# Kernel optimization log

Hardware: AMD Instinct MI355X
Metric: run time of the kernel (lower is better)

Reference implementation:

```python
import jax, jax.numpy as jnp
import numpy as np

B, N, D, OUT = 32, 4096, 512, 512
LN_EPS = 1e-5
EPS = 1e-8


def _layernorm(x, g, b):
    m = jnp.mean(x, axis=-1, keepdims=True)
    v = jnp.mean((x - m) ** 2, axis=-1, keepdims=True)
    return (x - m) * jax.lax.rsqrt(v + LN_EPS) * g + b


def setup_inputs() -> dict:
    key = jax.random.key(0)
    ks = jax.random.split(key, 12)
    x = jax.random.normal(ks[0], (B, N, D), dtype=jnp.float32)
    mask = jax.random.bernoulli(ks[1], 0.9, (B, N))
    mask = mask.at[:, 0].set(True)  # guarantee no fully-masked row
    h = D // 4
    s = lambda fan_in: 1.0 / np.sqrt(fan_in)
    return {
        "x": x,
        "mask": mask,
        # attention MLP: Linear(D, D//4) -> tanh -> Linear(D//4, 1)
        "attn_w1": jax.random.normal(ks[2], (D, h), jnp.float32) * s(D),
        "attn_b1": jnp.zeros((h,), jnp.float32),
        "attn_w2": jax.random.normal(ks[3], (h, 1), jnp.float32) * s(h),
        "attn_b2": jnp.zeros((1,), jnp.float32),
        # gate: Linear(3D, D) -> LN -> GELU -> Linear(D, 3) -> softmax
        "gate_w1": jax.random.normal(ks[4], (3 * D, D), jnp.float32) * s(3 * D),
        "gate_b1": jnp.zeros((D,), jnp.float32),
        "gate_ln_g": jnp.ones((D,), jnp.float32),
        "gate_ln_b": jnp.zeros((D,), jnp.float32),
        "gate_w2": jax.random.normal(ks[5], (D, 3), jnp.float32) * s(D),
        "gate_b2": jnp.zeros((3,), jnp.float32),
        # out_proj: Linear(D, OUT) -> LN -> Dropout(eval: identity)
        "out_w": jax.random.normal(ks[6], (D, OUT), jnp.float32) * s(D),
        "out_b": jnp.zeros((OUT,), jnp.float32),
        "out_ln_g": jnp.ones((OUT,), jnp.float32),
        "out_ln_b": jnp.zeros((OUT,), jnp.float32),
    }


def reference(x, mask, attn_w1, attn_b1, attn_w2, attn_b2,
              gate_w1, gate_b1, gate_ln_g, gate_ln_b, gate_w2, gate_b2,
              out_w, out_b, out_ln_g, out_ln_b):
    # attention scores: [B, N]
    h = jnp.tanh(jnp.einsum('bnd,dh->bnh', x, attn_w1) + attn_b1)
    scores = (jnp.einsum('bnh,ho->bno', h, attn_w2) + attn_b2)[..., 0]
    scores = jnp.where(mask, scores, -jnp.inf)
    attn_w = jax.nn.softmax(scores, axis=-1)
    attn_w = jnp.nan_to_num(attn_w, nan=0.0)
    attn_pooled = jnp.einsum('bnd,bn->bd', x, attn_w)

    # masked max pool
    x_masked = jnp.where(mask[..., None], x, -jnp.inf)
    max_pooled = jnp.max(x_masked, axis=1)
    max_pooled = jnp.nan_to_num(max_pooled, nan=0.0, posinf=0.0, neginf=0.0)

    # masked mean pool
    mfl = mask.astype(x.dtype)
    masked_sum = jnp.einsum('bnd,bn->bd', x, mfl)
    num_valid = jnp.clip(jnp.sum(mfl, axis=1, keepdims=True), EPS, None)
    mean_pooled = masked_sum / num_valid

    # gated combine
    combined = jnp.concatenate([attn_pooled, max_pooled, mean_pooled], axis=-1)
    g = combined @ gate_w1 + gate_b1
    g = _layernorm(g, gate_ln_g, gate_ln_b)
    g = jax.nn.gelu(g, approximate=False)
    gates = jax.nn.softmax(g @ gate_w2 + gate_b2, axis=-1)  # [B, 3]

    stacked = jnp.stack([attn_pooled, max_pooled, mean_pooled], axis=2)  # [B, D, 3]
    weighted = jnp.einsum('bdk,bk->bd', stacked, gates)

    out = weighted @ out_w + out_b
    out = _layernorm(out, out_ln_g, out_ln_b)  # dropout: eval mode -> identity
    return out
```

## Files before the change

### kernel.cpp

```cpp
#include <hip/hip_runtime.h>
#include <hip/hip_bf16.h>
#include <math.h>

#define BB 32
#define NN 4096
#define DD 512
#define HH 128
#define NCH 128
#define LN_EPS 1e-5f
#define MEPS 1e-8f

typedef __attribute__((ext_vector_type(8))) short bf16x8;
typedef __attribute__((ext_vector_type(4))) float f32x4;

__device__ __forceinline__ unsigned pk_bf16(float a, float b) {
    unsigned ua = __float_as_uint(a); ua = (ua + 0x7FFFu + ((ua >> 16) & 1u)) >> 16;
    unsigned ub = __float_as_uint(b); ub = (ub + 0x7FFFu + ((ub >> 16) & 1u)) >> 16;
    return ua | (ub << 16);
}
__device__ __forceinline__ unsigned short bf16_1(float a) {
    unsigned ua = __float_as_uint(a);
    return (unsigned short)((ua + 0x7FFFu + ((ua >> 16) & 1u)) >> 16);
}
__device__ __forceinline__ float bflo(unsigned u) { return __uint_as_float(u << 16); }
__device__ __forceinline__ float bfhi(unsigned u) { return __uint_as_float(u & 0xFFFF0000u); }

__global__ __launch_bounds__(256) void gmsp_prep(
    const void* __restrict__ mask, unsigned char* __restrict__ m8,
    const float* __restrict__ w1, unsigned short* __restrict__ w1f)
{
    int blk = blockIdx.x, t = threadIdx.x;
    if (blk < 512) {
        __shared__ int sf[2];
        const unsigned* mu = (const unsigned*)mask;
        bool f32f = false, i8f = false;
#pragma unroll
        for (int i = 0; i < 4; ++i) {
            unsigned v = mu[t + i * 256];
            f32f |= (v == 0x3F800000u);
            i8f  |= (v > 1u) && (v != 0x3F800000u);
        }
        if (t == 0) { sf[0] = 0; sf[1] = 0; }
        __syncthreads();
        int wf32 = __any((int)f32f), wi8 = __any((int)i8f);
        if ((t & 63) == 0) {
            if (wf32) atomicOr(&sf[0], 1);
            if (wi8)  atomicOr(&sf[1], 1);
        }
        __syncthreads();
        int fmt = sf[0] ? 2 : (sf[1] ? 1 : 0);
        int i = blk * 256 + t;
        unsigned char v;
        if (fmt == 1)      v = ((const unsigned char*)mask)[i] != 0;
        else if (fmt == 2) v = ((const float*)mask)[i] != 0.0f;
        else               v = ((const int*)mask)[i] != 0;
        m8[i] = v;
    } else {
        int idx = (blk - 512) * 256 + t;
        int j = idx & 7;
        int e = idx >> 3;
        int lane = e & 63;
        int half = (e >> 6) & 1;
        int s = (e >> 7) & 15;
        int g2 = (e >> 11) & 3;
        int h = g2 * 32 + half * 16 + (lane & 15);
        int k = s * 32 + (lane >> 4) * 8 + j;
        w1f[(size_t)e * 8 + j] = bf16_1(w1[(size_t)k * HH + h]);
    }
}

__global__ __launch_bounds__(256, 4) void gmsp_fused(
    const float* __restrict__ x, const unsigned short* __restrict__ w1f,
    const float* __restrict__ b1, const float* __restrict__ w2,
    const float* __restrict__ b2, const unsigned char* __restrict__ m8,
    float* __restrict__ attnp, float* __restrict__ sump, float* __restrict__ maxp,
    float* __restrict__ mc, float* __restrict__ sc, float* __restrict__ cnt)
{
    __shared__ char At[32 * 1024];
    __shared__ float sred[32][4] __attribute__((aligned(16)));
    __shared__ float wrow[32];
    __shared__ float cpool[2][512];

    const int t = threadIdx.x;
    const int lane = t & 63, wid = t >> 6;
    const int l15 = lane & 15, lq = (lane >> 4) & 3;
    const int blk = blockIdx.x;
    const int b = blk >> 7, ch = blk & 127;
    const size_t row0 = (size_t)b * NN + (size_t)ch * 32;

    float4 sreg[16];
    {
        const float4* xb = (const float4*)(x + row0 * DD);
#pragma unroll
        for (int j = 0; j < 16; ++j) sreg[j] = xb[j * 256 + t];
    }
    uint4 mq0 = *(const uint4*)(m8 + row0);
    uint4 mq1 = *(const uint4*)(m8 + row0 + 16);
    unsigned mwa[8] = {mq0.x, mq0.y, mq0.z, mq0.w, mq1.x, mq1.y, mq1.z, mq1.w};

    const int H = t >> 7;
    const int c4 = t & 127;
    float ps[4] = {0.f, 0.f, 0.f, 0.f};
    float pm[4] = {-INFINITY, -INFINITY, -INFINITY, -INFINITY};
#pragma unroll
    for (int j = 0; j < 16; ++j) {
        const int row = 2 * j + H;
        float4 v = sreg[j];
        uint2 pw; pw.x = pk_bf16(v.x, v.y); pw.y = pk_bf16(v.z, v.w);
        *(uint2*)(At + row * 1024 + ((c4 * 8) ^ ((row & 7) << 4))) = pw;
        int mv = (mwa[j >> 1] >> ((2 * (j & 1) + H) * 8)) & 0xFF;
        if (mv) {
            ps[0] += v.x; ps[1] += v.y; ps[2] += v.z; ps[3] += v.w;
            pm[0] = fmaxf(pm[0], v.x); pm[1] = fmaxf(pm[1], v.y);
            pm[2] = fmaxf(pm[2], v.z); pm[3] = fmaxf(pm[3], v.w);
        }
    }
    __syncthreads();

    const int hb = wid * 32;
    f32x4 acc00 = (f32x4)0.f, acc01 = (f32x4)0.f, acc10 = (f32x4)0.f, acc11 = (f32x4)0.f;
    {
        const char* wf = (const char*)w1f + (size_t)wid * 32768 + (size_t)lane * 16;
        const char* ar0 = At + l15 * 1024;
        const char* ar1 = At + (16 + l15) * 1024;
        const int swz = (l15 & 7) << 4;
#pragma unroll
        for (int s = 0; s < 16; ++s) {
            bf16x8 bf0 = *(const bf16x8*)(wf + s * 2048);
            bf16x8 bf1 = *(const bf16x8*)(wf + s * 2048 + 1024);
            const int co = (s * 64 + lq * 16) ^ swz;
            bf16x8 a0 = *(const bf16x8*)(ar0 + co);
            bf16x8 a1 = *(const bf16x8*)(ar1 + co);
            acc00 = __builtin_amdgcn_mfma_f32_16x16x32_bf16(a0, bf0, acc00, 0, 0, 0);
            acc01 = __builtin_amdgcn_mfma_f32_16x16x32_bf16(a0, bf1, acc01, 0, 0, 0);
            acc10 = __builtin_amdgcn_mfma_f32_16x16x32_bf16(a1, bf0, acc10, 0, 0, 0);
            acc11 = __builtin_amdgcn_mfma_f32_16x16x32_bf16(a1, bf1, acc11, 0, 0, 0);
        }
    }
    {
        const float b10 = b1[hb + l15], b11 = b1[hb + 16 + l15];
        const float w20 = w2[hb + l15], w21 = w2[hb + 16 + l15];
#pragma unroll
        for (int rf = 0; rf < 2; ++rf) {
            f32x4 aA = rf ? acc10 : acc00;
            f32x4 aB = rf ? acc11 : acc01;
#pragma unroll
            for (int r = 0; r < 4; ++r) {
                float p0 = fminf(fmaxf(aA[r] + b10, -10.f), 10.f);
                float p1 = fminf(fmaxf(aB[r] + b11, -10.f), 10.f);
                float e0 = __expf(2.f * p0), e1 = __expf(2.f * p1);
                float v = (e0 - 1.f) / (e0 + 1.f) * w20 + (e1 - 1.f) / (e1 + 1.f) * w21;
                v += __shfl_xor(v, 1); v += __shfl_xor(v, 2);
                v += __shfl_xor(v, 4); v += __shfl_xor(v, 8);
                if (l15 == 0) sred[rf * 16 + lq * 4 + r][wid] = v;
            }
        }
    }
    __syncthreads();

    if (t < 32) {
        float4 s4 = *(const float4*)&sred[t][0];
        float ssum = s4.x + s4.y + s4.z + s4.w + b2[0];
        int valid = m8[row0 + t];
        float score = valid ? ssum : -INFINITY;
        float mx = score;
        mx = fmaxf(mx, __shfl_xor(mx, 1));  mx = fmaxf(mx, __shfl_xor(mx, 2));
        mx = fmaxf(mx, __shfl_xor(mx, 4));  mx = fmaxf(mx, __shfl_xor(mx, 8));
        mx = fmaxf(mx, __shfl_xor(mx, 16));
        float e = valid ? __expf(score - mx) : 0.f;
        wrow[t] = e;
        float ts = e, tc = valid ? 1.f : 0.f;
        ts += __shfl_xor(ts, 1);  tc += __shfl_xor(tc, 1);
        ts += __shfl_xor(ts, 2);  tc += __shfl_xor(tc, 2);
        ts += __shfl_xor(ts, 4);  tc += __shfl_xor(tc, 4);
        ts += __shfl_xor(ts, 8);  tc += __shfl_xor(tc, 8);
        ts += __shfl_xor(ts, 16); tc += __shfl_xor(tc, 16);
        if (t == 0) { mc[blk] = mx; sc[blk] = ts; cnt[blk] = tc; }
    }
    __syncthreads();

    float a0 = 0.f, a1 = 0.f;
#pragma unroll 8
    for (int r = 0; r < 32; ++r) {
        float w = wrow[r];
        unsigned u = *(const unsigned*)(At + r * 1024 + ((t * 4) ^ ((r & 7) << 4)));
        a0 = fmaf(w, bflo(u), a0);
        a1 = fmaf(w, bfhi(u), a1);
    }

    *(float4*)&cpool[H][c4 * 4] = make_float4(ps[0], ps[1], ps[2], ps[3]);
    __syncthreads();
    float sv0 = cpool[0][2 * t] + cpool[1][2 * t];
    float sv1 = cpool[0][2 * t + 1] + cpool[1][2 * t + 1];
    __syncthreads();
    *(float4*)&cpool[H][c4 * 4] = make_float4(pm[0], pm[1], pm[2], pm[3]);
    __syncthreads();
    float mv0 = fmaxf(cpool[0][2 * t], cpool[1][2 * t]);
    float mv1 = fmaxf(cpool[0][2 * t + 1], cpool[1][2 * t + 1]);

    const size_t ob = (size_t)blk * DD + 2 * t;
    *(float2*)(attnp + ob) = make_float2(a0, a1);
    *(float2*)(sump + ob)  = make_float2(sv0, sv1);
    *(float2*)(maxp + ob)  = make_float2(mv0, mv1);
}

__device__ __forceinline__ float gmsp_bsum(float v, float* red, int t) {
    __syncthreads();
    red[t] = v; __syncthreads();
    for (int s = 256; s > 0; s >>= 1) { if (t < s) red[t] += red[t + s]; __syncthreads(); }
    return red[0];
}
__device__ __forceinline__ float gmsp_bmax(float v, float* red, int t) {
    __syncthreads();
    red[t] = v; __syncthreads();
    for (int s = 256; s > 0; s >>= 1) { if (t < s) red[t] = fmaxf(red[t], red[t + s]); __syncthreads(); }
    return red[0];
}

__global__ __launch_bounds__(512) void gmsp_tail(
    const float* __restrict__ attnp, const float* __restrict__ sump,
    const float* __restrict__ maxp, const float* __restrict__ mc,
    const float* __restrict__ sc, const float* __restrict__ cnt,
    const float* __restrict__ gate_w1, const float* __restrict__ gate_b1,
    const float* __restrict__ gln_g, const float* __restrict__ gln_b,
    const float* __restrict__ gate_w2, const float* __restrict__ gate_b2,
    const float* __restrict__ out_w, const float* __restrict__ out_b,
    const float* __restrict__ oln_g, const float* __restrict__ oln_b,
    float* __restrict__ out)
{
    __shared__ float comb[3 * DD];
    __shared__ float wvec[DD];
    __shared__ float red[512];
    __shared__ float ef[NCH];
    __shared__ float part[4][DD];
    int b = blockIdx.x, t = threadIdx.x;

    float mcv = (t < NCH) ? mc[b * NCH + t] : -INFINITY;
    float M = gmsp_bmax(mcv, red, t);
    float e = (t < NCH && mcv != -INFINITY) ? __expf(mcv - M) : 0.f;
    if (t < NCH) ef[t] = e;
    float T = gmsp_bsum(e * ((t < NCH) ? sc[b * NCH + t] : 0.f), red, t);
    float C = gmsp_bsum((t < NCH) ? cnt[b * NCH + t] : 0.f, red, t);
    float invT = T > 0.f ? 1.f / T : 0.f;
    C = fmaxf(C, MEPS);
    __syncthreads();

    float ax = 0.f, sx = 0.f, mx = -INFINITY;
    for (int c = 0; c < NCH; ++c) {
        size_t base = (size_t)(b * NCH + c) * DD + t;
        ax = fmaf(ef[c], attnp[base], ax);
        sx += sump[base];
        mx = fmaxf(mx, maxp[base]);
    }
    ax *= invT;
    float meanx = sx / C;
    if (isinf(mx)) mx = 0.f;

    comb[t] = ax;
    comb[DD + t] = mx;
    comb[2 * DD + t] = meanx;
    __syncthreads();

    const int th = t & 127, kh = t >> 7;
    {
        float4 g4 = make_float4(0.f, 0.f, 0.f, 0.f);
        const float* gw = gate_w1 + (size_t)kh * 384 * DD + th * 4;
        for (int k = 0; k < 384; ++k) {
            float cv = comb[kh * 384 + k];
            float4 wv = *(const float4*)(gw + (size_t)k * DD);
            g4.x = fmaf(cv, wv.x, g4.x); g4.y = fmaf(cv, wv.y, g4.y);
            g4.z = fmaf(cv, wv.z, g4.z); g4.w = fmaf(cv, wv.w, g4.w);
        }
        *(float4*)&part[kh][th * 4] = g4;
    }
    __syncthreads();
    float gx = part[0][t] + part[1][t] + part[2][t] + part[3][t] + gate_b1[t];

    float mg = gmsp_bsum(gx, red, t) * (1.f / DD);
    float vg = gmsp_bsum(gx * gx, red, t) * (1.f / DD) - mg * mg;
    float inv = rsqrtf(vg + LN_EPS);
    gx = (gx - mg) * inv * gln_g[t] + gln_b[t];
    gx = 0.5f * gx * (1.f + erff(gx * 0.70710678118654752f));

    float l0 = gmsp_bsum(gx * gate_w2[t * 3 + 0], red, t) + gate_b2[0];
    float l1 = gmsp_bsum(gx * gate_w2[t * 3 + 1], red, t) + gate_b2[1];
    float l2 = gmsp_bsum(gx * gate_w2[t * 3 + 2], red, t) + gate_b2[2];
    float mxl = fmaxf(l0, fmaxf(l1, l2));
    float e0 = __expf(l0 - mxl), e1 = __expf(l1 - mxl), e2 = __expf(l2 - mxl);
    float ie = 1.f / (e0 + e1 + e2);
    float gw0 = e0 * ie, gw1 = e1 * ie, gw2 = e2 * ie;

    wvec[t] = ax * gw0 + mx * gw1 + meanx * gw2;
    __syncthreads();

    {
        float4 o4 = make_float4(0.f, 0.f, 0.f, 0.f);
        const float* ow = out_w + (size_t)kh * 128 * DD + th * 4;
        for (int k = 0; k < 128; ++k) {
            float wvk = wvec[kh * 128 + k];
            float4 w4 = *(const float4*)(ow + (size_t)k * DD);
            o4.x = fmaf(wvk, w4.x, o4.x); o4.y = fmaf(wvk, w4.y, o4.y);
            o4.z = fmaf(wvk, w4.z, o4.z); o4.w = fmaf(wvk, w4.w, o4.w);
        }
        *(float4*)&part[kh][th * 4] = o4;
    }
    __syncthreads();
    float ox = part[0][t] + part[1][t] + part[2][t] + part[3][t] + out_b[t];

    float mo = gmsp_bsum(ox, red, t) * (1.f / DD);
    float vo = gmsp_bsum(ox * ox, red, t) * (1.f / DD) - mo * mo;
    float io = rsqrtf(vo + LN_EPS);
    out[(size_t)b * DD + t] = (ox - mo) * io * oln_g[t] + oln_b[t];
}

extern "C" void kernel_launch(void* const* d_in, const int* in_sizes, int n_in,
                              void* d_out, int out_size, void* d_ws, size_t ws_size,
                              hipStream_t stream) {
    const float* x        = (const float*)d_in[0];
    const void*  mask     = d_in[1];
    const float* attn_w1  = (const float*)d_in[2];
    const float* attn_b1  = (const float*)d_in[3];
    const float* attn_w2  = (const float*)d_in[4];
    const float* attn_b2  = (const float*)d_in[5];
    const float* gate_w1  = (const float*)d_in[6];
    const float* gate_b1  = (const float*)d_in[7];
    const float* gln_g    = (const float*)d_in[8];
    const float* gln_b    = (const float*)d_in[9];
    const float* gate_w2  = (const float*)d_in[10];
    const float* gate_b2  = (const float*)d_in[11];
    const float* out_w    = (const float*)d_in[12];
    const float* out_b    = (const float*)d_in[13];
    const float* oln_g    = (const float*)d_in[14];
    const float* oln_b    = (const float*)d_in[15];
    float* out = (float*)d_out;

    char* p = (char*)d_ws;
    unsigned char* m8 = (unsigned char*)p;      p += (size_t)BB * NN;
    unsigned short* w1f = (unsigned short*)p;   p += (size_t)DD * HH * 2;
    float* attnp = (float*)p;                   p += (size_t)BB * NCH * DD * 4;
    float* sump = (float*)p;                    p += (size_t)BB * NCH * DD * 4;
    float* maxp = (float*)p;                    p += (size_t)BB * NCH * DD * 4;
    float* mc = (float*)p;                      p += (size_t)BB * NCH * 4;
    float* sc = (float*)p;                      p += (size_t)BB * NCH * 4;
    float* cnt = (float*)p;                     p += (size_t)BB * NCH * 4;

    gmsp_prep<<<768, 256, 0, stream>>>(mask, m8, attn_w1, w1f);
    gmsp_fused<<<BB * NCH, 256, 0, stream>>>(x, w1f, attn_b1, attn_w2, attn_b2, m8,
                                             attnp, sump, maxp, mc, sc, cnt);
    gmsp_tail<<<BB, 512, 0, stream>>>(attnp, sump, maxp, mc, sc, cnt,
                                      gate_w1, gate_b1, gln_g, gln_b, gate_w2, gate_b2,
                                      out_w, out_b, oln_g, oln_b, out);
}
```

Measured before the change: 141.2 us.

## Halve LDS tile and re-read x from cache for pooling to raise occupancy

The fused kernel now stages x into LDS in two 256-column halves (16KB instead of 32KB) and drops the 64-register sreg buffer. It also raises launch bounds to 8 blocks per CU. Pooling (attention-weighted sum, masked sum and max) now re-reads x from global/L2 in full fp32 per row, using ballot and shuffle instead of the LDS wrow/cpool reductions. The goal is higher occupancy and fewer LDS round trips. The cost is a second pass over x through the cache and extra syncs between halves.

```diff
diff --git a/kernel.cpp b/kernel.cpp
--- a/kernel.cpp
+++ b/kernel.cpp
@@ -22,8 +22,6 @@
     unsigned ua = __float_as_uint(a);
     return (unsigned short)((ua + 0x7FFFu + ((ua >> 16) & 1u)) >> 16);
 }
-__device__ __forceinline__ float bflo(unsigned u) { return __uint_as_float(u << 16); }
-__device__ __forceinline__ float bfhi(unsigned u) { return __uint_as_float(u & 0xFFFF0000u); }
 
 __global__ __launch_bounds__(256) void gmsp_prep(
     const void* __restrict__ mask, unsigned char* __restrict__ m8,
@@ -69,17 +67,15 @@
     }
 }
 
-__global__ __launch_bounds__(256, 4) void gmsp_fused(
+__global__ __launch_bounds__(256, 8) void gmsp_fused(
     const float* __restrict__ x, const unsigned short* __restrict__ w1f,
     const float* __restrict__ b1, const float* __restrict__ w2,
     const float* __restrict__ b2, const unsigned char* __restrict__ m8,
     float* __restrict__ attnp, float* __restrict__ sump, float* __restrict__ maxp,
     float* __restrict__ mc, float* __restrict__ sc, float* __restrict__ cnt)
 {
-    __shared__ char At[32 * 1024];
+    __shared__ char At[16 * 1024];
     __shared__ float sred[32][4] __attribute__((aligned(16)));
-    __shared__ float wrow[32];
-    __shared__ float cpool[2][512];
 
     const int t = threadIdx.x;
     const int lane = t & 63, wid = t >> 6;
@@ -88,47 +84,32 @@
     const int b = blk >> 7, ch = blk & 127;
     const size_t row0 = (size_t)b * NN + (size_t)ch * 32;
 
-    float4 sreg[16];
-    {
-        const float4* xb = (const float4*)(x + row0 * DD);
-#pragma unroll
-        for (int j = 0; j < 16; ++j) sreg[j] = xb[j * 256 + t];
-    }
-    uint4 mq0 = *(const uint4*)(m8 + row0);
-    uint4 mq1 = *(const uint4*)(m8 + row0 + 16);
-    unsigned mwa[8] = {mq0.x, mq0.y, mq0.z, mq0.w, mq1.x, mq1.y, mq1.z, mq1.w};
-
-    const int H = t >> 7;
-    const int c4 = t & 127;
-    float ps[4] = {0.f, 0.f, 0.f, 0.f};
-    float pm[4] = {-INFINITY, -INFINITY, -INFINITY, -INFINITY};
-#pragma unroll
-    for (int j = 0; j < 16; ++j) {
-        const int row = 2 * j + H;
-        float4 v = sreg[j];
-        uint2 pw; pw.x = pk_bf16(v.x, v.y); pw.y = pk_bf16(v.z, v.w);
-        *(uint2*)(At + row * 1024 + ((c4 * 8) ^ ((row & 7) << 4))) = pw;
-        int mv = (mwa[j >> 1] >> ((2 * (j & 1) + H) * 8)) & 0xFF;
-        if (mv) {
-            ps[0] += v.x; ps[1] += v.y; ps[2] += v.z; ps[3] += v.w;
-            pm[0] = fmaxf(pm[0], v.x); pm[1] = fmaxf(pm[1], v.y);
-            pm[2] = fmaxf(pm[2], v.z); pm[3] = fmaxf(pm[3], v.w);
-        }
-    }
-    __syncthreads();
-
-    const int hb = wid * 32;
+    const char* wf = (const char*)w1f + (size_t)wid * 32768 + (size_t)lane * 16;
+    const int swz = (l15 & 7) << 4;
+    const char* ar0 = At + l15 * 512;
+    const char* ar1 = At + (16 + l15) * 512;
+
     f32x4 acc00 = (f32x4)0.f, acc01 = (f32x4)0.f, acc10 = (f32x4)0.f, acc11 = (f32x4)0.f;
-    {
-        const char* wf = (const char*)w1f + (size_t)wid * 32768 + (size_t)lane * 16;
-        const char* ar0 = At + l15 * 1024;
-        const char* ar1 = At + (16 + l15) * 1024;
-        const int swz = (l15 & 7) << 4;
-#pragma unroll
-        for (int s = 0; s < 16; ++s) {
+
+#pragma unroll
+    for (int h = 0; h < 2; ++h) {
+#pragma unroll
+        for (int j = 0; j < 8; ++j) {
+            const int idx = j * 256 + t;
+            const int row = idx >> 6;
+            const int c64 = idx & 63;
+            float4 v = *(const float4*)(x + (row0 + row) * DD + h * 256 + c64 * 4);
+            uint2 pw; pw.x = pk_bf16(v.x, v.y); pw.y = pk_bf16(v.z, v.w);
+            *(uint2*)(At + row * 512 + ((c64 * 8) ^ ((row & 7) << 4))) = pw;
+        }
+        __syncthreads();
+
+#pragma unroll
+        for (int sp = 0; sp < 8; ++sp) {
+            const int s = h * 8 + sp;
             bf16x8 bf0 = *(const bf16x8*)(wf + s * 2048);
             bf16x8 bf1 = *(const bf16x8*)(wf + s * 2048 + 1024);
-            const int co = (s * 64 + lq * 16) ^ swz;
+            const int co = (sp * 64 + lq * 16) ^ swz;
             bf16x8 a0 = *(const bf16x8*)(ar0 + co);
             bf16x8 a1 = *(const bf16x8*)(ar1 + co);
             acc00 = __builtin_amdgcn_mfma_f32_16x16x32_bf16(a0, bf0, acc00, 0, 0, 0);
@@ -136,10 +117,12 @@
             acc10 = __builtin_amdgcn_mfma_f32_16x16x32_bf16(a1, bf0, acc10, 0, 0, 0);
             acc11 = __builtin_amdgcn_mfma_f32_16x16x32_bf16(a1, bf1, acc11, 0, 0, 0);
         }
-    }
+        __syncthreads();
+    }
+
     {
-        const float b10 = b1[hb + l15], b11 = b1[hb + 16 + l15];
-        const float w20 = w2[hb + l15], w21 = w2[hb + 16 + l15];
+        const float b10 = b1[wid * 32 + l15], b11 = b1[wid * 32 + 16 + l15];
+        const float w20 = w2[wid * 32 + l15], w21 = w2[wid * 32 + 16 + l15];
 #pragma unroll
         for (int rf = 0; rf < 2; ++rf) {
             f32x4 aA = rf ? acc10 : acc00;
@@ -158,50 +141,46 @@
     }
     __syncthreads();
 
-    if (t < 32) {
-        float4 s4 = *(const float4*)&sred[t][0];
-        float ssum = s4.x + s4.y + s4.z + s4.w + b2[0];
-        int valid = m8[row0 + t];
-        float score = valid ? ssum : -INFINITY;
+    float wv; unsigned mb;
+    {
+        const int rl = lane & 31;
+        float4 s4 = *(const float4*)&sred[rl][0];
+        float ssc = s4.x + s4.y + s4.z + s4.w + b2[0];
+        bool val = m8[row0 + rl] != 0;
+        mb = (unsigned)__ballot((int)val);
+        float score = val ? ssc : -INFINITY;
         float mx = score;
         mx = fmaxf(mx, __shfl_xor(mx, 1));  mx = fmaxf(mx, __shfl_xor(mx, 2));
         mx = fmaxf(mx, __shfl_xor(mx, 4));  mx = fmaxf(mx, __shfl_xor(mx, 8));
         mx = fmaxf(mx, __shfl_xor(mx, 16));
-        float e = valid ? __expf(score - mx) : 0.f;
-        wrow[t] = e;
-        float ts = e, tc = valid ? 1.f : 0.f;
-        ts += __shfl_xor(ts, 1);  tc += __shfl_xor(tc, 1);
-        ts += __shfl_xor(ts, 2);  tc += __shfl_xor(tc, 2);
-        ts += __shfl_xor(ts, 4);  tc += __shfl_xor(tc, 4);
-        ts += __shfl_xor(ts, 8);  tc += __shfl_xor(tc, 8);
-        ts += __shfl_xor(ts, 16); tc += __shfl_xor(tc, 16);
-        if (t == 0) { mc[blk] = mx; sc[blk] = ts; cnt[blk] = tc; }
-    }
-    __syncthreads();
-
-    float a0 = 0.f, a1 = 0.f;
+        wv = val ? __expf(score - mx) : 0.f;
+        float ts = wv;
+        ts += __shfl_xor(ts, 1); ts += __shfl_xor(ts, 2);
+        ts += __shfl_xor(ts, 4); ts += __shfl_xor(ts, 8);
+        ts += __shfl_xor(ts, 16);
+        if (t == 0) {
+            mc[blk] = mx; sc[blk] = ts;
+            cnt[blk] = (float)__builtin_popcount(mb);
+        }
+    }
+
+    const float* xb = x + row0 * DD + 2 * t;
+    float a0 = 0.f, a1 = 0.f, s0 = 0.f, s1 = 0.f;
+    float m0 = -INFINITY, m1 = -INFINITY;
 #pragma unroll 8
     for (int r = 0; r < 32; ++r) {
-        float w = wrow[r];
-        unsigned u = *(const unsigned*)(At + r * 1024 + ((t * 4) ^ ((r & 7) << 4)));
-        a0 = fmaf(w, bflo(u), a0);
-        a1 = fmaf(w, bfhi(u), a1);
-    }
-
-    *(float4*)&cpool[H][c4 * 4] = make_float4(ps[0], ps[1], ps[2], ps[3]);
-    __syncthreads();
-    float sv0 = cpool[0][2 * t] + cpool[1][2 * t];
-    float sv1 = cpool[0][2 * t + 1] + cpool[1][2 * t + 1];
-    __syncthreads();
-    *(float4*)&cpool[H][c4 * 4] = make_float4(pm[0], pm[1], pm[2], pm[3]);
-    __syncthreads();
-    float mv0 = fmaxf(cpool[0][2 * t], cpool[1][2 * t]);
-    float mv1 = fmaxf(cpool[0][2 * t + 1], cpool[1][2 * t + 1]);
-
+        float2 v = *(const float2*)(xb + (size_t)r * DD);
+        float w = __shfl(wv, r);
+        a0 = fmaf(w, v.x, a0); a1 = fmaf(w, v.y, a1);
+        if (mb & (1u << r)) {
+            s0 += v.x; s1 += v.y;
+            m0 = fmaxf(m0, v.x); m1 = fmaxf(m1, v.y);
+        }
+    }
     const size_t ob = (size_t)blk * DD + 2 * t;
     *(float2*)(attnp + ob) = make_float2(a0, a1);
-    *(float2*)(sump + ob)  = make_float2(sv0, sv1);
-    *(float2*)(maxp + ob)  = make_float2(mv0, mv1);
+    *(float2*)(sump + ob)  = make_float2(s0, s1);
+    *(float2*)(maxp + ob)  = make_float2(m0, m1);
 }
 
 __device__ __forceinline__ float gmsp_bsum(float v, float* red, int t) {
```

After: 204.9 us. +45.1%, slower.
